# Optimization experiments

Measured on AMD Instinct MI355X. Metric: run time of the kernel, lower is better.

The kernel has to match this reference:

```python
import jax, jax.numpy as jnp
import numpy as np
import math

B, L, D, H = 2, 2048, 1024, 16
HD = D // H

def setup_inputs() -> dict:
    key = jax.random.key(0)
    ks = jax.random.split(key, 8)
    s = 1.0 / math.sqrt(D)
    # causal additive mask: 0 on/below diagonal, -inf above
    causal = jnp.where(jnp.tril(jnp.ones((L, L), dtype=bool)), 0.0, -jnp.inf)
    causal = causal[None, None].astype(jnp.float32)  # [1,1,L,L]
    return {
        "Q": jax.random.normal(ks[0], (B, L, D), jnp.float32),
        "K": jax.random.normal(ks[1], (B, L, D), jnp.float32),
        "V": jax.random.normal(ks[2], (B, L, D), jnp.float32),
        "attn_mask": causal,
        "padding_mask": jnp.zeros((B, L), dtype=bool),
        "wq": jax.random.normal(ks[3], (D, D), jnp.float32) * s,
        "wk": jax.random.normal(ks[4], (D, D), jnp.float32) * s,
        "wv": jax.random.normal(ks[5], (D, D), jnp.float32) * s,
        "wout": jax.random.normal(ks[6], (D, D), jnp.float32) * s,
    }

def reference(Q, K, V, attn_mask, padding_mask, wq, wk, wv, wout):
    b, l, _ = Q.shape
    # projections (torch Linear: x @ W.T); weights sampled as [out,in]-like square
    def proj(x, w):
        return (x @ w.T).reshape(b, l, H, HD).transpose(0, 2, 1, 3)  # [B,H,L,hd]
    q = proj(Q, wq)
    k = proj(K, wk)
    v = proj(V, wv)
    scores = jnp.einsum("bhqd,bhkd->bhqk", q, k) / math.sqrt(HD)
    scores = scores + attn_mask
    scores = jnp.where(padding_mask[:, None, None, :], -jnp.inf, scores)
    weights = jax.nn.softmax(scores, axis=-1)
    ctx = jnp.einsum("bhqk,bhkd->bhqd", weights, v)
    ctx = ctx.transpose(0, 2, 1, 3).reshape(b, l, D)
    return ctx @ wout.T
```

## Files before the change

### kernel.cpp

```cpp
#include <hip/hip_runtime.h>
#include <stdint.h>
#include <stddef.h>

typedef __bf16 bf16_t;
typedef bf16_t bf16x4 __attribute__((ext_vector_type(4)));
typedef bf16_t bf16x8 __attribute__((ext_vector_type(8)));
typedef float f32x4 __attribute__((ext_vector_type(4)));

#define MFMA_BF16(A_, B_, C_) __builtin_amdgcn_mfma_f32_16x16x32_bf16(A_, B_, C_, 0, 0, 0)

static constexpr int Lseq = 2048;
static constexpr int Dmod = 1024;
static constexpr int Hn   = 16;
static constexpr int HDim = 64;
static constexpr size_t M1 = 1u << 20;

__device__ __forceinline__ int swz(int row, int chunk) {
  return row * 64 + ((chunk ^ (row & 7)) << 3);
}

__device__ __forceinline__ void async_ld16(const bf16_t* g, bf16_t* l) {
  __builtin_amdgcn_global_load_lds(
      (const __attribute__((address_space(1))) void*)g,
      (__attribute__((address_space(3))) void*)l, 16, 0, 0);
}

__global__ __launch_bounds__(256) void cvt_kernel(
    const float* __restrict__ Q, const float* __restrict__ K,
    const float* __restrict__ V, const float* __restrict__ wq,
    const float* __restrict__ wk, const float* __restrict__ wv,
    const float* __restrict__ wout, bf16_t* __restrict__ wsb)
{
  const int s = blockIdx.z;
  const float* __restrict__ src;
  if      (s < 4)   src = Q    + (size_t)s * M1;
  else if (s < 8)   src = K    + (size_t)(s - 4) * M1;
  else if (s < 12)  src = V    + (size_t)(s - 8) * M1;
  else if (s == 12) src = wq;
  else if (s == 13) src = wk;
  else if (s == 14) src = wv;
  else              src = wout;
  bf16_t* __restrict__ dst = wsb + (size_t)s * M1;

  const int idx = blockIdx.x * 256 + threadIdx.x;
  float4 a = ((const float4*)src)[idx * 2];
  float4 b = ((const float4*)src)[idx * 2 + 1];
  bf16x8 o;
  o[0] = (bf16_t)a.x; o[1] = (bf16_t)a.y; o[2] = (bf16_t)a.z; o[3] = (bf16_t)a.w;
  o[4] = (bf16_t)b.x; o[5] = (bf16_t)b.y; o[6] = (bf16_t)b.z; o[7] = (bf16_t)b.w;
  ((bf16x8*)dst)[idx] = o;
}

__global__ __launch_bounds__(256) void proj_kernel(
    const bf16_t* __restrict__ Qbf, const bf16_t* __restrict__ Kbf,
    const bf16_t* __restrict__ Vbf, const bf16_t* __restrict__ wqb,
    const bf16_t* __restrict__ wkb, const bf16_t* __restrict__ wvb,
    bf16_t* __restrict__ qo, bf16_t* __restrict__ ko, bf16_t* __restrict__ vo)
{
  const int z = blockIdx.z;
  const bf16_t* __restrict__ A  = (z == 0) ? Qbf : (z == 1) ? Kbf : Vbf;
  const bf16_t* __restrict__ Bw = (z == 0) ? wqb : (z == 1) ? wkb : wvb;
  bf16_t* __restrict__ dst      = (z == 0) ? qo  : (z == 1) ? ko  : vo;

  __shared__ __align__(16) bf16_t As[128 * 64];
  __shared__ __align__(16) bf16_t Bs[64 * 64];

  const int tid  = threadIdx.x;
  const int wave = tid >> 6;
  const int lane = tid & 63;
  const int quad = lane >> 4;
  const int l16  = lane & 15;
  const int wm   = (wave & 1) * 64;
  const int wn   = (wave >> 1) * 32;
  const int n0   = blockIdx.x * 64;
  const int m0   = blockIdx.y * 128;

  const int srow8  = lane >> 3;
  const int schunk = (lane & 7) ^ srow8;

  f32x4 acc[4][2];
#pragma unroll
  for (int i = 0; i < 4; ++i)
#pragma unroll
    for (int j = 0; j < 2; ++j)
#pragma unroll
      for (int e = 0; e < 4; ++e) acc[i][j][e] = 0.0f;

  for (int kt = 0; kt < 16; ++kt) {
    const int k0 = kt * 64;
    __syncthreads();
#pragma unroll
    for (int i = 0; i < 4; ++i) {
      const int rb = wave * 32 + i * 8;
      async_ld16(&A[(size_t)(m0 + rb + srow8) * Dmod + k0 + schunk * 8], &As[rb * 64]);
    }
#pragma unroll
    for (int i = 0; i < 2; ++i) {
      const int rb = wave * 16 + i * 8;
      async_ld16(&Bw[(size_t)(n0 + rb + srow8) * Dmod + k0 + schunk * 8], &Bs[rb * 64]);
    }
    __syncthreads();

    bf16x8 af[4][2], bfr[2][2];
#pragma unroll
    for (int mt = 0; mt < 4; ++mt) {
      const int row = wm + mt * 16 + l16;
      af[mt][0] = *(const bf16x8*)&As[swz(row, quad)];
      af[mt][1] = *(const bf16x8*)&As[swz(row, quad + 4)];
    }
#pragma unroll
    for (int nt = 0; nt < 2; ++nt) {
      const int row = wn + nt * 16 + l16;
      bfr[nt][0] = *(const bf16x8*)&Bs[swz(row, quad)];
      bfr[nt][1] = *(const bf16x8*)&Bs[swz(row, quad + 4)];
    }
#pragma unroll
    for (int mt = 0; mt < 4; ++mt)
#pragma unroll
      for (int nt = 0; nt < 2; ++nt) {
        acc[mt][nt] = MFMA_BF16(af[mt][0], bfr[nt][0], acc[mt][nt]);
        acc[mt][nt] = MFMA_BF16(af[mt][1], bfr[nt][1], acc[mt][nt]);
      }
  }

#pragma unroll
  for (int mt = 0; mt < 4; ++mt) {
    const int grb = m0 + wm + mt * 16 + quad * 4;
    const int bb  = grb >> 11;
    const int lb  = grb & 2047;
#pragma unroll
    for (int nt = 0; nt < 2; ++nt) {
      const int gc = n0 + wn + nt * 16 + l16;
      const int h  = gc >> 6;
      const int hd = gc & 63;
      if (z == 2) {
        bf16x4 pk;
#pragma unroll
        for (int r = 0; r < 4; ++r) pk[r] = (bf16_t)acc[mt][nt][r];
        *(bf16x4*)&dst[(((size_t)(bb * Hn + h) * HDim + hd) << 11) + lb] = pk;
      } else {
#pragma unroll
        for (int r = 0; r < 4; ++r)
          dst[(((size_t)(bb * Hn + h) * Lseq + lb + r) << 6) + hd] = (bf16_t)acc[mt][nt][r];
      }
    }
  }
}

__global__ __launch_bounds__(512) void attn_kernel(
    const bf16_t* __restrict__ q, const bf16_t* __restrict__ k,
    const bf16_t* __restrict__ v, bf16_t* __restrict__ ctx)
{
  const int px = blockIdx.x;
  const int bh = blockIdx.y;
  const int bb = bh >> 4;
  const int h  = bh & 15;

  const int tid  = threadIdx.x;
  const int wave = tid >> 6;
  const int lane = tid & 63;
  const int quad = lane >> 4;
  const int l16  = lane & 15;

  __shared__ __align__(16) bf16_t Ks[2][64 * 64];
  __shared__ __align__(16) bf16_t Vs[2][64 * 64];
  __shared__ __align__(16) bf16_t Ps[8][16][72];

  const bf16_t* __restrict__ qb = q + (size_t)bh * (Lseq * HDim);
  const bf16_t* __restrict__ kb = k + (size_t)bh * (Lseq * HDim);
  const bf16_t* __restrict__ vb = v + (size_t)bh * (HDim * Lseq);

  const int srow8  = lane >> 3;
  const int schunk = (lane & 7) ^ srow8;
  const int rb     = wave * 8;

  bf16x8 ones;
#pragma unroll
  for (int i = 0; i < 8; ++i) ones[i] = (bf16_t)1.0f;

  for (int half = 0; half < 2; ++half) {
    const int qblk = half ? (15 - px) : px;
    const int q0   = qblk * 128;
    const int qrow = q0 + wave * 16 + l16;

    bf16x8 qf0 = *(const bf16x8*)&qb[(size_t)qrow * HDim + quad * 8];
    bf16x8 qf1 = *(const bf16x8*)&qb[(size_t)qrow * HDim + 32 + quad * 8];

    f32x4 o[4];
    f32x4 lacc;
#pragma unroll
    for (int e = 0; e < 4; ++e) lacc[e] = 0.0f;
#pragma unroll
    for (int nt = 0; nt < 4; ++nt)
#pragma unroll
      for (int e = 0; e < 4; ++e) o[nt][e] = 0.0f;

    __syncthreads();
    async_ld16(&kb[(size_t)(rb + srow8) * HDim + schunk * 8], &Ks[0][rb * 64]);
    async_ld16(&vb[(size_t)(rb + srow8) * Lseq + schunk * 8], &Vs[0][rb * 64]);

    const int njt = 2 * qblk + 2;
    const int diag_start = 2 * qblk + (wave >> 2);
    for (int jt = 0; jt < njt; ++jt) {
      const int cur = jt & 1;
      __syncthreads();

      if (jt + 1 < njt) {
        const int j1 = (jt + 1) * 64;
        async_ld16(&kb[(size_t)(j1 + rb + srow8) * HDim + schunk * 8], &Ks[cur ^ 1][rb * 64]);
        async_ld16(&vb[(size_t)(rb + srow8) * Lseq + j1 + schunk * 8], &Vs[cur ^ 1][rb * 64]);
      }

      const int j0 = jt * 64;
      f32x4 s[4];
#pragma unroll
      for (int nt = 0; nt < 4; ++nt) {
#pragma unroll
        for (int e = 0; e < 4; ++e) s[nt][e] = 0.0f;
        const int krow = nt * 16 + l16;
        bf16x8 kf0 = *(const bf16x8*)&Ks[cur][swz(krow, quad)];
        bf16x8 kf1 = *(const bf16x8*)&Ks[cur][swz(krow, quad + 4)];
        s[nt] = MFMA_BF16(kf0, qf0, s[nt]);
        s[nt] = MFMA_BF16(kf1, qf1, s[nt]);
      }

      const bool need_mask = (jt >= diag_start);
#pragma unroll
      for (int nt = 0; nt < 4; ++nt) {
        bf16x4 pk;
#pragma unroll
        for (int r = 0; r < 4; ++r) {
          float val = s[nt][r] * 0.18033688f;
          if (need_mask && (j0 + nt * 16 + quad * 4 + r > qrow)) val = -1e30f;
          pk[r] = (bf16_t)__builtin_amdgcn_exp2f(val);
        }
        *(bf16x4*)&Ps[wave][l16][nt * 16 + quad * 4] = pk;
      }

      bf16x8 pf0 = *(const bf16x8*)&Ps[wave][l16][quad * 8];
      bf16x8 pf1 = *(const bf16x8*)&Ps[wave][l16][32 + quad * 8];

      lacc = MFMA_BF16(pf0, ones, lacc);
      lacc = MFMA_BF16(pf1, ones, lacc);

#pragma unroll
      for (int nt = 0; nt < 4; ++nt) {
        const int vrow = nt * 16 + l16;
        bf16x8 vf0 = *(const bf16x8*)&Vs[cur][swz(vrow, quad)];
        bf16x8 vf1 = *(const bf16x8*)&Vs[cur][swz(vrow, quad + 4)];
        o[nt] = MFMA_BF16(pf0, vf0, o[nt]);
        o[nt] = MFMA_BF16(pf1, vf1, o[nt]);
      }
    }

    float inv[4];
#pragma unroll
    for (int r = 0; r < 4; ++r) inv[r] = 1.0f / lacc[r];
#pragma unroll
    for (int nt = 0; nt < 4; ++nt)
#pragma unroll
      for (int r = 0; r < 4; ++r) {
        const int gq = q0 + wave * 16 + quad * 4 + r;
        ctx[(size_t)(bb * Lseq + gq) * Dmod + h * HDim + nt * 16 + l16] =
            (bf16_t)(o[nt][r] * inv[r]);
      }
  }
}

__global__ __launch_bounds__(256) void out_kernel(
    const bf16_t* __restrict__ Actx, const bf16_t* __restrict__ Bwout,
    float* __restrict__ out)
{
  __shared__ __align__(16) bf16_t As[128 * 64];
  __shared__ __align__(16) bf16_t Bs[64 * 64];

  const int tid  = threadIdx.x;
  const int wave = tid >> 6;
  const int lane = tid & 63;
  const int quad = lane >> 4;
  const int l16  = lane & 15;
  const int wm   = (wave & 1) * 64;
  const int wn   = (wave >> 1) * 32;
  const int n0   = blockIdx.x * 64;
  const int m0   = blockIdx.y * 128;

  const int srow8  = lane >> 3;
  const int schunk = (lane & 7) ^ srow8;

  f32x4 acc[4][2];
#pragma unroll
  for (int i = 0; i < 4; ++i)
#pragma unroll
    for (int j = 0; j < 2; ++j)
#pragma unroll
      for (int e = 0; e < 4; ++e) acc[i][j][e] = 0.0f;

  for (int kt = 0; kt < 16; ++kt) {
    const int k0 = kt * 64;
    __syncthreads();
#pragma unroll
    for (int i = 0; i < 4; ++i) {
      const int rb = wave * 32 + i * 8;
      async_ld16(&Actx[(size_t)(m0 + rb + srow8) * Dmod + k0 + schunk * 8], &As[rb * 64]);
    }
#pragma unroll
    for (int i = 0; i < 2; ++i) {
      const int rb = wave * 16 + i * 8;
      async_ld16(&Bwout[(size_t)(n0 + rb + srow8) * Dmod + k0 + schunk * 8], &Bs[rb * 64]);
    }
    __syncthreads();

    bf16x8 af[4][2], bfr[2][2];
#pragma unroll
    for (int mt = 0; mt < 4; ++mt) {
      const int row = wm + mt * 16 + l16;
      af[mt][0] = *(const bf16x8*)&As[swz(row, quad)];
      af[mt][1] = *(const bf16x8*)&As[swz(row, quad + 4)];
    }
#pragma unroll
    for (int nt = 0; nt < 2; ++nt) {
      const int row = wn + nt * 16 + l16;
      bfr[nt][0] = *(const bf16x8*)&Bs[swz(row, quad)];
      bfr[nt][1] = *(const bf16x8*)&Bs[swz(row, quad + 4)];
    }
#pragma unroll
    for (int mt = 0; mt < 4; ++mt)
#pragma unroll
      for (int nt = 0; nt < 2; ++nt) {
        acc[mt][nt] = MFMA_BF16(af[mt][0], bfr[nt][0], acc[mt][nt]);
        acc[mt][nt] = MFMA_BF16(af[mt][1], bfr[nt][1], acc[mt][nt]);
      }
  }

#pragma unroll
  for (int mt = 0; mt < 4; ++mt) {
    const int grb = m0 + wm + mt * 16 + quad * 4;
#pragma unroll
    for (int nt = 0; nt < 2; ++nt) {
      const int gc = n0 + wn + nt * 16 + l16;
#pragma unroll
      for (int r = 0; r < 4; ++r)
        out[(size_t)(grb + r) * Dmod + gc] = acc[mt][nt][r];
    }
  }
}

extern "C" void kernel_launch(void* const* d_in, const int* in_sizes, int n_in,
                              void* d_out, int out_size, void* d_ws, size_t ws_size,
                              hipStream_t stream) {
  (void)in_sizes; (void)n_in; (void)out_size; (void)ws_size;
  const float* Q    = (const float*)d_in[0];
  const float* K    = (const float*)d_in[1];
  const float* V    = (const float*)d_in[2];
  const float* wq   = (const float*)d_in[5];
  const float* wk   = (const float*)d_in[6];
  const float* wv   = (const float*)d_in[7];
  const float* wout = (const float*)d_in[8];
  float* out = (float*)d_out;

  bf16_t* wsb = (bf16_t*)d_ws;
  bf16_t* Qbf   = wsb;
  bf16_t* Kbf   = wsb + 4 * M1;
  bf16_t* Vbf   = wsb + 8 * M1;
  bf16_t* wqb   = wsb + 12 * M1;
  bf16_t* wkb   = wsb + 13 * M1;
  bf16_t* wvb   = wsb + 14 * M1;
  bf16_t* woutb = wsb + 15 * M1;
  bf16_t* qp    = wsb + 16 * M1;
  bf16_t* kp    = wsb + 20 * M1;
  bf16_t* vp    = wsb + 24 * M1;
  bf16_t* cws   = wsb;

  cvt_kernel<<<dim3(512, 1, 16), 256, 0, stream>>>(Q, K, V, wq, wk, wv, wout, wsb);
  proj_kernel<<<dim3(16, 32, 3), 256, 0, stream>>>(Qbf, Kbf, Vbf, wqb, wkb, wvb, qp, kp, vp);
  attn_kernel<<<dim3(8, 32), 512, 0, stream>>>(qp, kp, vp, cws);
  out_kernel<<<dim3(16, 32), 256, 0, stream>>>(cws, woutb, out);
}
```

Measured before the change: 225.5 us.

## Shrink attention blocks to 64-row tiles, fold softmax scale into wq, reorder grids

The attention kernel now uses 256-thread blocks over 64-query tiles, paired as qt and 31-qt for causal load balance. This doubles the number of blocks and means only the single diagonal key tile needs masking. The softmax scale (1/sqrt(64)*log2e) is folded into the bf16 conversion of wq, which removes a multiply per score element. The grid indexing of the projection, output and attention kernels is swapped so consecutive blocks share the same weight column tile or the same head, which may improve L2 locality. Rounding wq to bf16 after scaling slightly changes numerics.

Result: faster. 213.7 us (-5.2%).

```diff
diff --git a/kernel.cpp b/kernel.cpp
--- a/kernel.cpp
+++ b/kernel.cpp
@@ -41,13 +41,16 @@
   else if (s == 14) src = wv;
   else              src = wout;
   bf16_t* __restrict__ dst = wsb + (size_t)s * M1;
+  const float scale = (s == 12) ? 0.18033688f : 1.0f;
 
   const int idx = blockIdx.x * 256 + threadIdx.x;
   float4 a = ((const float4*)src)[idx * 2];
   float4 b = ((const float4*)src)[idx * 2 + 1];
   bf16x8 o;
-  o[0] = (bf16_t)a.x; o[1] = (bf16_t)a.y; o[2] = (bf16_t)a.z; o[3] = (bf16_t)a.w;
-  o[4] = (bf16_t)b.x; o[5] = (bf16_t)b.y; o[6] = (bf16_t)b.z; o[7] = (bf16_t)b.w;
+  o[0] = (bf16_t)(a.x * scale); o[1] = (bf16_t)(a.y * scale);
+  o[2] = (bf16_t)(a.z * scale); o[3] = (bf16_t)(a.w * scale);
+  o[4] = (bf16_t)(b.x * scale); o[5] = (bf16_t)(b.y * scale);
+  o[6] = (bf16_t)(b.z * scale); o[7] = (bf16_t)(b.w * scale);
   ((bf16x8*)dst)[idx] = o;
 }
 
@@ -72,8 +75,8 @@
   const int l16  = lane & 15;
   const int wm   = (wave & 1) * 64;
   const int wn   = (wave >> 1) * 32;
-  const int n0   = blockIdx.x * 64;
-  const int m0   = blockIdx.y * 128;
+  const int m0   = blockIdx.x * 128;
+  const int n0   = blockIdx.y * 64;
 
   const int srow8  = lane >> 3;
   const int schunk = (lane & 7) ^ srow8;
@@ -147,12 +150,12 @@
   }
 }
 
-__global__ __launch_bounds__(512) void attn_kernel(
+__global__ __launch_bounds__(256) void attn_kernel(
     const bf16_t* __restrict__ q, const bf16_t* __restrict__ k,
     const bf16_t* __restrict__ v, bf16_t* __restrict__ ctx)
 {
-  const int px = blockIdx.x;
-  const int bh = blockIdx.y;
+  const int bh = blockIdx.x;
+  const int px = blockIdx.y;
   const int bb = bh >> 4;
   const int h  = bh & 15;
 
@@ -164,7 +167,7 @@
 
   __shared__ __align__(16) bf16_t Ks[2][64 * 64];
   __shared__ __align__(16) bf16_t Vs[2][64 * 64];
-  __shared__ __align__(16) bf16_t Ps[8][16][72];
+  __shared__ __align__(16) bf16_t Ps[4][16][72];
 
   const bf16_t* __restrict__ qb = q + (size_t)bh * (Lseq * HDim);
   const bf16_t* __restrict__ kb = k + (size_t)bh * (Lseq * HDim);
@@ -172,15 +175,14 @@
 
   const int srow8  = lane >> 3;
   const int schunk = (lane & 7) ^ srow8;
-  const int rb     = wave * 8;
 
   bf16x8 ones;
 #pragma unroll
   for (int i = 0; i < 8; ++i) ones[i] = (bf16_t)1.0f;
 
   for (int half = 0; half < 2; ++half) {
-    const int qblk = half ? (15 - px) : px;
-    const int q0   = qblk * 128;
+    const int qt = half ? (31 - px) : px;
+    const int q0 = qt * 64;
     const int qrow = q0 + wave * 16 + l16;
 
     bf16x8 qf0 = *(const bf16x8*)&qb[(size_t)qrow * HDim + quad * 8];
@@ -196,22 +198,29 @@
       for (int e = 0; e < 4; ++e) o[nt][e] = 0.0f;
 
     __syncthreads();
-    async_ld16(&kb[(size_t)(rb + srow8) * HDim + schunk * 8], &Ks[0][rb * 64]);
-    async_ld16(&vb[(size_t)(rb + srow8) * Lseq + schunk * 8], &Vs[0][rb * 64]);
-
-    const int njt = 2 * qblk + 2;
-    const int diag_start = 2 * qblk + (wave >> 2);
-    for (int jt = 0; jt < njt; ++jt) {
+#pragma unroll
+    for (int i = 0; i < 2; ++i) {
+      const int rb = wave * 16 + i * 8;
+      const int r  = rb + srow8;
+      async_ld16(&kb[(size_t)r * HDim + schunk * 8], &Ks[0][rb * 64]);
+      async_ld16(&vb[(size_t)r * Lseq + schunk * 8], &Vs[0][rb * 64]);
+    }
+
+    for (int jt = 0; jt <= qt; ++jt) {
       const int cur = jt & 1;
       __syncthreads();
 
-      if (jt + 1 < njt) {
+      if (jt < qt) {
         const int j1 = (jt + 1) * 64;
-        async_ld16(&kb[(size_t)(j1 + rb + srow8) * HDim + schunk * 8], &Ks[cur ^ 1][rb * 64]);
-        async_ld16(&vb[(size_t)(rb + srow8) * Lseq + j1 + schunk * 8], &Vs[cur ^ 1][rb * 64]);
-      }
-
-      const int j0 = jt * 64;
+#pragma unroll
+        for (int i = 0; i < 2; ++i) {
+          const int rb = wave * 16 + i * 8;
+          const int r  = rb + srow8;
+          async_ld16(&kb[(size_t)(j1 + r) * HDim + schunk * 8], &Ks[cur ^ 1][rb * 64]);
+          async_ld16(&vb[(size_t)r * Lseq + j1 + schunk * 8], &Vs[cur ^ 1][rb * 64]);
+        }
+      }
+
       f32x4 s[4];
 #pragma unroll
       for (int nt = 0; nt < 4; ++nt) {
@@ -224,14 +233,14 @@
         s[nt] = MFMA_BF16(kf1, qf1, s[nt]);
       }
 
-      const bool need_mask = (jt >= diag_start);
+      const bool diag = (jt == qt);
 #pragma unroll
       for (int nt = 0; nt < 4; ++nt) {
         bf16x4 pk;
 #pragma unroll
         for (int r = 0; r < 4; ++r) {
-          float val = s[nt][r] * 0.18033688f;
-          if (need_mask && (j0 + nt * 16 + quad * 4 + r > qrow)) val = -1e30f;
+          float val = s[nt][r];
+          if (diag && (nt * 16 + quad * 4 + r > wave * 16 + l16)) val = -1e30f;
           pk[r] = (bf16_t)__builtin_amdgcn_exp2f(val);
         }
         *(bf16x4*)&Ps[wave][l16][nt * 16 + quad * 4] = pk;
@@ -281,8 +290,8 @@
   const int l16  = lane & 15;
   const int wm   = (wave & 1) * 64;
   const int wn   = (wave >> 1) * 32;
-  const int n0   = blockIdx.x * 64;
-  const int m0   = blockIdx.y * 128;
+  const int m0   = blockIdx.x * 128;
+  const int n0   = blockIdx.y * 64;
 
   const int srow8  = lane >> 3;
   const int schunk = (lane & 7) ^ srow8;
@@ -372,7 +381,7 @@
   bf16_t* cws   = wsb;
 
   cvt_kernel<<<dim3(512, 1, 16), 256, 0, stream>>>(Q, K, V, wq, wk, wv, wout, wsb);
-  proj_kernel<<<dim3(16, 32, 3), 256, 0, stream>>>(Qbf, Kbf, Vbf, wqb, wkb, wvb, qp, kp, vp);
-  attn_kernel<<<dim3(8, 32), 512, 0, stream>>>(qp, kp, vp, cws);
-  out_kernel<<<dim3(16, 32), 256, 0, stream>>>(cws, woutb, out);
-}
+  proj_kernel<<<dim3(32, 16, 3), 256, 0, stream>>>(Qbf, Kbf, Vbf, wqb, wkb, wvb, qp, kp, vp);
+  attn_kernel<<<dim3(32, 16), 256, 0, stream>>>(qp, kp, vp, cws);
+  out_kernel<<<dim3(32, 16), 256, 0, stream>>>(cws, woutb, out);
+}
```
